# Kernel optimization log

Measured on AMD Instinct MI355X. Metric: run time of the kernel, lower is better.

The kernel has to match this reference:

```python
import jax, jax.numpy as jnp
from jax import lax
import numpy as np

B, C_IN, C_OUT, T, N, E = 4, 32, 32, 48, 2000, 16000


def _tconv(x, w, b):
    # Conv2d with kernel (3,1), padding (1,0): temporal conv over T, per-node.
    y = lax.conv_general_dilated(x, w, window_strides=(1, 1),
                                 padding=((1, 1), (0, 0)),
                                 dimension_numbers=('NCHW', 'OIHW', 'NCHW'))
    return y + b[None, :, None, None]


def setup_inputs() -> dict:
    key = jax.random.key(0)
    ks = jax.random.split(key, 8)
    x = jax.random.normal(ks[0], (B, C_IN, T, N), dtype=jnp.float32)
    edge_index = jax.random.randint(ks[1], (2, E), 0, N, dtype=jnp.int64)
    w1 = jax.random.normal(ks[2], (C_OUT, C_IN, 3, 1), dtype=jnp.float32) * 0.05
    b1 = jnp.zeros((C_OUT,), dtype=jnp.float32)
    gcn_w = jax.random.normal(ks[3], (C_OUT, C_OUT), dtype=jnp.float32) * 0.05
    gcn_b = jnp.zeros((C_OUT,), dtype=jnp.float32)
    w2 = jax.random.normal(ks[4], (C_OUT, C_OUT, 3, 1), dtype=jnp.float32) * 0.05
    b2 = jnp.zeros((C_OUT,), dtype=jnp.float32)
    return {"x": x, "edge_index": edge_index, "w1": w1, "b1": b1,
            "gcn_w": gcn_w, "gcn_b": gcn_b, "w2": w2, "b2": b2}


def reference(x, edge_index, w1, b1, gcn_w, gcn_b, w2, b2):
    # temporal conv 1 + relu
    h = jax.nn.relu(_tconv(x, w1, b1))          # [B, C, T, N]
    Bs, C, Ts, Ns = h.shape
    # replicate-graph GCN: same edge_index for all B*T graphs
    xf = h.transpose(0, 2, 3, 1).reshape(Bs * Ts, Ns, C)   # [BT, N, C]
    xw = xf @ gcn_w                                        # linear transform first
    src, dst = edge_index[0], edge_index[1]
    # GCN symmetric normalization with self-loops: deg = 1 + in-degree
    deg = jnp.zeros((Ns,), xw.dtype).at[dst].add(1.0) + 1.0
    dinv = lax.rsqrt(deg)
    wedge = dinv[src] * dinv[dst]                           # [E]

    def aggregate(g):  # g: [N, C] for one graph
        return jnp.zeros((Ns, C), g.dtype).at[dst].add(g[src] * wedge[:, None])

    agg = jax.vmap(aggregate)(xw)                           # [BT, N, C]
    out = agg + (1.0 / deg)[None, :, None] * xw + gcn_b     # self-loop term + bias
    out = out.reshape(Bs, Ts, Ns, C).transpose(0, 3, 1, 2)  # [B, C, T, N]
    # temporal conv 2
    return _tconv(out, w2, b2)
```

## Files before the change

kernel.cpp:

```cpp
#include <hip/hip_runtime.h>

#define BB 4
#define CIN 32
#define COUT 32
#define TT 48
#define NN 2000
#define EE 16000
#define BT (BB*TT)
#define PADCOL 24576


__global__ __launch_bounds__(1024) void k_build(
        const int* __restrict__ ei,
        const float* __restrict__ w1, const float* __restrict__ gw,
        const float* __restrict__ gb, const float* __restrict__ w2,
        int* __restrict__ rowptr, float* __restrict__ dinv2,
        float* __restrict__ dinvg, int* __restrict__ fillptr,
        int* __restrict__ col, float* __restrict__ wedge,
        float* __restrict__ w1t, float* __restrict__ w2c,
        float* __restrict__ bias2) {
    __shared__ int   cnt[2048];
    __shared__ int   buf[2048];
    __shared__ float sw2t[3072];
    __shared__ float sgw[1024];
    int t = threadIdx.x;

    for (int i = t; i < 3072; i += 1024) {
        int c = i & 31, r = i >> 5;
        int co = r & 31, k = r >> 5;
        sw2t[i] = w2[c * 96 + co * 3 + k];
        w1t[i]  = w1[c * 96 + co * 3 + k];
    }
    sgw[t] = gw[t];
    cnt[t] = 0; cnt[t + 1024] = 0;
    __syncthreads();

    for (int e = t; e < EE; e += 1024) atomicAdd(&cnt[ei[EE + e]], 1);
    __syncthreads();

    for (int i = t; i < 2048; i += 1024)
        buf[i] = (i < NN) ? ((cnt[i] + 3) & ~3) : 0;
    __syncthreads();
    for (int s = 1; s < 2048; s <<= 1) {
        int i0 = t, i1 = t + 1024;
        int a0 = buf[i0] + ((i0 >= s) ? buf[i0 - s] : 0);
        int a1 = buf[i1] + ((i1 >= s) ? buf[i1 - s] : 0);
        __syncthreads();
        buf[i0] = a0; buf[i1] = a1;
        __syncthreads();
    }

    for (int i = t; i < 2048; i += 1024) {
        if (i < NN) {
            rowptr[i + 1] = buf[i];
            float deg = (float)(cnt[i] + 1);
            dinvg[i] = rsqrtf(deg);
            dinv2[i] = 1.0f / deg;
            fillptr[i] = buf[i] - ((cnt[i] + 3) & ~3);
        }
    }
    if (t == 0) rowptr[0] = 0;

    int P = buf[NN - 1];
    __syncthreads();
    for (int i = t; i < P; i += 1024) { col[i] = 0; wedge[i] = 0.f; }

    for (int i = t; i < 3072; i += 1024) {
        int c = i & 31, r = i >> 5;
        int cm = r & 31, k = r >> 5;
        float acc = 0.f;
#pragma unroll
        for (int co = 0; co < 32; co++)
            acc += sgw[cm * 32 + co] * sw2t[(k * 32 + co) * 32 + c];
        w2c[i] = acc;
    }
    for (int i = t; i < 96; i += 1024) {
        int k = i >> 5, c = i & 31;
        float acc = 0.f;
#pragma unroll
        for (int co = 0; co < 32; co++)
            acc += gb[co] * sw2t[(k * 32 + co) * 32 + c];
        bias2[i] = acc;
    }
}


__global__ void k_fill(const int* __restrict__ ei, int* __restrict__ fillptr,
                       const float* __restrict__ dinvg,
                       int* __restrict__ col, float* __restrict__ wedge) {
    int e = blockIdx.x * blockDim.x + threadIdx.x;
    if (e < EE) {
        int s = ei[e], d = ei[EE + e];
        int pos = atomicAdd(fillptr + d, 1);
        col[pos]   = s;
        wedge[pos] = dinvg[s] * dinvg[d];
    }
}


__global__ __launch_bounds__(256) void k_conv1(const float* __restrict__ x,
                                               const float* __restrict__ w1t,
                                               const float* __restrict__ b1,
                                               float* __restrict__ hbuf) {
    int bid = blockIdx.x;
    int xcd = bid & 7;
    int i   = bid >> 3;
    int nch = i & 7;
    int r   = i >> 3;
    int tloc = r % 6, b = r / 6;
    int t = xcd * 6 + tloc;
    int n = nch * 256 + threadIdx.x;
    if (n >= NN) return;
    int g = b * TT + t;
    int gb = g >> 3, gsub = g & 7;

    float ha[COUT];
#pragma unroll
    for (int c = 0; c < COUT; c++) ha[c] = b1[c];

    for (int k = 0; k < 3; k++) {
        int tt = t + k - 1;
        if (tt < 0 || tt >= TT) continue;
        const float* xb = x + (((size_t)b * CIN) * TT + tt) * NN + n;

        float xv[CIN];
#pragma unroll
        for (int ci = 0; ci < CIN; ci++)
            xv[ci] = xb[(size_t)ci * TT * NN];
        __builtin_amdgcn_sched_barrier(0);

        const float* wp = w1t + k * CIN * COUT;
#pragma unroll
        for (int ci = 0; ci < CIN; ci++) {
#pragma unroll
            for (int c = 0; c < COUT; c++) ha[c] += xv[ci] * wp[ci * COUT + c];
        }
        __builtin_amdgcn_sched_barrier(0);
    }

    float4* pa = (float4*)(hbuf + (((size_t)gb * NN + n) * 8 + gsub) * 32);
#pragma unroll
    for (int q = 0; q < 8; q++)
        pa[q] = make_float4(fmaxf(ha[4*q], 0.f), fmaxf(ha[4*q+1], 0.f),
                            fmaxf(ha[4*q+2], 0.f), fmaxf(ha[4*q+3], 0.f));
}


__global__ __launch_bounds__(256) void k_agg(const float* __restrict__ hbuf,
                                             const int* __restrict__ rowptr,
                                             const int* __restrict__ col,
                                             const float* __restrict__ wedge,
                                             const float* __restrict__ dinv2,
                                             float* __restrict__ gbuf) {
    int bid = blockIdx.x;
    int xcd = bid & 7;
    int q   = bid >> 3;
    int gbr = q / 500;
    int nch = q % 500;
    int gb  = gbr * 8 + xcd;
    int wid  = threadIdx.x >> 6;
    int lane = threadIdx.x & 63;
    int gsub = lane >> 3;
    int cq   = lane & 7;
    int n    = nch * 4 + wid;

    const float* xg = hbuf + (size_t)gb * NN * 256;
    size_t loff = (size_t)gsub * 32 + cq * 4;

    float4 self = *(const float4*)(xg + (size_t)n * 256 + loff);
    float dv = dinv2[n];
    float4 acc = make_float4(dv * self.x, dv * self.y, dv * self.z, dv * self.w);

    int j  = rowptr[n];
    int je = rowptr[n + 1];
    for (; j < je; j += 4) {
        int4   cc = *(const int4*)(col + j);
        float4 ww = *(const float4*)(wedge + j);
        float4 v0 = *(const float4*)(xg + (size_t)cc.x * 256 + loff);
        float4 v1 = *(const float4*)(xg + (size_t)cc.y * 256 + loff);
        float4 v2 = *(const float4*)(xg + (size_t)cc.z * 256 + loff);
        float4 v3 = *(const float4*)(xg + (size_t)cc.w * 256 + loff);
        acc.x += ww.x*v0.x + ww.y*v1.x + ww.z*v2.x + ww.w*v3.x;
        acc.y += ww.x*v0.y + ww.y*v1.y + ww.z*v2.y + ww.w*v3.y;
        acc.z += ww.x*v0.z + ww.y*v1.z + ww.z*v2.z + ww.w*v3.z;
        acc.w += ww.x*v0.w + ww.y*v1.w + ww.z*v2.w + ww.w*v3.w;
    }

    int g = gb * 8 + gsub;
    *(float4*)(gbuf + ((size_t)g * NN + n) * 32 + cq * 4) = acc;
}


__global__ __launch_bounds__(256) void k_conv2(const float* __restrict__ gbuf,
                                               const float* __restrict__ w2c,
                                               const float* __restrict__ bias2,
                                               const float* __restrict__ b2,
                                               float* __restrict__ out) {
    int n = blockIdx.x * 256 + threadIdx.x;
    if (n >= NN) return;
    int t = blockIdx.y, b = blockIdx.z;

    float o[COUT];
#pragma unroll
    for (int c = 0; c < COUT; c++) o[c] = b2[c];

    for (int k = 0; k < 3; k++) {
        int tt = t + k - 1;
        if (tt < 0 || tt >= TT) continue;
        const float4* gp = (const float4*)(gbuf + (((size_t)(b * TT + tt)) * NN + n) * CIN);
        const float* wp = w2c + k * CIN * COUT;
        const float* bp = bias2 + k * COUT;
        float gv[CIN];
#pragma unroll
        for (int qq = 0; qq < 8; qq++) {
            float4 v = gp[qq];
            gv[4*qq] = v.x; gv[4*qq+1] = v.y; gv[4*qq+2] = v.z; gv[4*qq+3] = v.w;
        }
#pragma unroll
        for (int c = 0; c < COUT; c++) o[c] += bp[c];
#pragma unroll
        for (int cm = 0; cm < CIN; cm++) {
#pragma unroll
            for (int c = 0; c < COUT; c++) o[c] += gv[cm] * wp[cm * COUT + c];
        }
    }

#pragma unroll
    for (int c = 0; c < COUT; c++)
        out[(((size_t)b * COUT + c) * TT + t) * NN + n] = o[c];
}


extern "C" void kernel_launch(void* const* d_in, const int* in_sizes, int n_in,
                              void* d_out, int out_size, void* d_ws, size_t ws_size,
                              hipStream_t stream) {
    const float* x     = (const float*)d_in[0];
    const int*   ei    = (const int*)d_in[1];
    const float* w1    = (const float*)d_in[2];
    const float* b1    = (const float*)d_in[3];
    const float* gcn_w = (const float*)d_in[4];
    const float* gcn_b = (const float*)d_in[5];
    const float* w2    = (const float*)d_in[6];
    const float* b2    = (const float*)d_in[7];
    float* out = (float*)d_out;

    const size_t XWB = (size_t)BT * NN * COUT * sizeof(float);
    char* w = (char*)d_ws;
    float* hbuf    = (float*)w;  w += XWB;
    float* gbuf    = (float*)w;  w += XWB;
    int*   rowptr  = (int*)w;    w += 8192;
    float* dinv2   = (float*)w;  w += 8192;
    float* dinvg   = (float*)w;  w += 8192;
    int*   fillptr = (int*)w;    w += 8192;
    int*   col     = (int*)w;    w += PADCOL * sizeof(int);
    float* wedge   = (float*)w;  w += PADCOL * sizeof(float);
    float* w1t     = (float*)w;  w += 3072 * sizeof(float);
    float* w2c     = (float*)w;  w += 3072 * sizeof(float);
    float* bias2   = (float*)w;  w += 96 * sizeof(float);

    k_build<<<dim3(1), dim3(1024), 0, stream>>>(ei, w1, gcn_w, gcn_b, w2,
                                                rowptr, dinv2, dinvg, fillptr,
                                                col, wedge, w1t, w2c, bias2);
    k_fill <<<dim3((EE + 255) / 256), dim3(256), 0, stream>>>(ei, fillptr, dinvg, col, wedge);
    k_conv1<<<dim3(1536), dim3(256), 0, stream>>>(x, w1t, b1, hbuf);
    k_agg  <<<dim3(12000), dim3(256), 0, stream>>>(hbuf, rowptr, col, wedge, dinv2, gbuf);
    k_conv2<<<dim3(8, TT, BB), dim3(256), 0, stream>>>(gbuf, w2c, bias2, b2, out);
}
```

Baseline: 248.4 us.

## Compute two output timesteps per thread in conv2 with shared tap loads

Each conv2 thread now produces two adjacent output timesteps, so the four gbuf input timesteps are loaded once and reused across both outputs instead of loading three taps per output. Bias contributions are precomputed into three boundary classes in k_build, and the grid is flattened with an XCD-aware block mapping plus sched_barriers to interleave loads and FMAs. This cuts gbuf traffic by about a third, at the cost of higher register pressure from two 32-wide accumulators and two 32-wide input buffers.

```diff
diff --git a/kernel.cpp b/kernel.cpp
--- a/kernel.cpp
+++ b/kernel.cpp
@@ -14,15 +14,17 @@
         const int* __restrict__ ei,
         const float* __restrict__ w1, const float* __restrict__ gw,
         const float* __restrict__ gb, const float* __restrict__ w2,
+        const float* __restrict__ cb2,
         int* __restrict__ rowptr, float* __restrict__ dinv2,
         float* __restrict__ dinvg, int* __restrict__ fillptr,
         int* __restrict__ col, float* __restrict__ wedge,
         float* __restrict__ w1t, float* __restrict__ w2c,
-        float* __restrict__ bias2) {
+        float* __restrict__ biasE) {
     __shared__ int   cnt[2048];
     __shared__ int   buf[2048];
     __shared__ float sw2t[3072];
     __shared__ float sgw[1024];
+    __shared__ float sbk[96];
     int t = threadIdx.x;
 
     for (int i = t; i < 3072; i += 1024) {
@@ -80,7 +82,15 @@
 #pragma unroll
         for (int co = 0; co < 32; co++)
             acc += gb[co] * sw2t[(k * 32 + co) * 32 + c];
-        bias2[i] = acc;
+        sbk[i] = acc;
+    }
+    __syncthreads();
+    for (int i = t; i < 96; i += 1024) {
+        int cls = i >> 5, c = i & 31;
+        float v = cb2[c] + sbk[32 + c];
+        if (cls != 0) v += sbk[c];
+        if (cls != 2) v += sbk[64 + c];
+        biasE[i] = v;
     }
 }
 
@@ -191,43 +201,79 @@
 }
 
 
-__global__ __launch_bounds__(256) void k_conv2(const float* __restrict__ gbuf,
-                                               const float* __restrict__ w2c,
-                                               const float* __restrict__ bias2,
-                                               const float* __restrict__ b2,
-                                               float* __restrict__ out) {
-    int n = blockIdx.x * 256 + threadIdx.x;
+#define LOADTAP(GV, TIDX) { \
+    const float4* gp_ = (const float4*)(gbuf + (((size_t)(b * TT + (TIDX))) * NN + n) * 32); \
+    _Pragma("unroll") \
+    for (int q_ = 0; q_ < 8; q_++) { \
+        float4 v_ = gp_[q_]; \
+        GV[4*q_] = v_.x; GV[4*q_+1] = v_.y; GV[4*q_+2] = v_.z; GV[4*q_+3] = v_.w; } }
+
+#define KBLK(ACC, GV, WP) { \
+    _Pragma("unroll") \
+    for (int cm_ = 0; cm_ < 32; cm_++) { \
+        float g_ = GV[cm_]; \
+        _Pragma("unroll") \
+        for (int c_ = 0; c_ < 32; c_++) ACC[c_] += g_ * (WP)[cm_ * 32 + c_]; } }
+
+#define STOREACC(ACC, TOUT, BP) { \
+    _Pragma("unroll") \
+    for (int c_ = 0; c_ < 32; c_++) \
+        out[(((size_t)b * COUT + c_) * TT + (TOUT)) * NN + n] = ACC[c_] + (BP)[c_]; }
+
+__global__ __launch_bounds__(256, 3) void k_conv2(const float* __restrict__ gbuf,
+                                                  const float* __restrict__ w2c,
+                                                  const float* __restrict__ biasE,
+                                                  float* __restrict__ out) {
+    int bid  = blockIdx.x;
+    int xcd  = bid & 7;
+    int slot = bid >> 3;
+    int grp  = xcd * 12 + (slot >> 3);
+    int nch  = slot & 7;
+    int b  = grp / 24;
+    int tc = grp % 24;
+    int t0 = tc * 2;
+    int n  = nch * 256 + threadIdx.x;
     if (n >= NN) return;
-    int t = blockIdx.y, b = blockIdx.z;
-
-    float o[COUT];
-#pragma unroll
-    for (int c = 0; c < COUT; c++) o[c] = b2[c];
-
-    for (int k = 0; k < 3; k++) {
-        int tt = t + k - 1;
-        if (tt < 0 || tt >= TT) continue;
-        const float4* gp = (const float4*)(gbuf + (((size_t)(b * TT + tt)) * NN + n) * CIN);
-        const float* wp = w2c + k * CIN * COUT;
-        const float* bp = bias2 + k * COUT;
-        float gv[CIN];
-#pragma unroll
-        for (int qq = 0; qq < 8; qq++) {
-            float4 v = gp[qq];
-            gv[4*qq] = v.x; gv[4*qq+1] = v.y; gv[4*qq+2] = v.z; gv[4*qq+3] = v.w;
-        }
-#pragma unroll
-        for (int c = 0; c < COUT; c++) o[c] += bp[c];
-#pragma unroll
-        for (int cm = 0; cm < CIN; cm++) {
-#pragma unroll
-            for (int c = 0; c < COUT; c++) o[c] += gv[cm] * wp[cm * COUT + c];
-        }
-    }
-
-#pragma unroll
-    for (int c = 0; c < COUT; c++)
-        out[(((size_t)b * COUT + c) * TT + t) * NN + n] = o[c];
+
+    const float* W0 = w2c;
+    const float* W1 = w2c + 1024;
+    const float* W2 = w2c + 2048;
+
+    float acc0[COUT], acc1[COUT];
+#pragma unroll
+    for (int c = 0; c < COUT; c++) { acc0[c] = 0.f; acc1[c] = 0.f; }
+
+    float ga[CIN], gbv[CIN];
+
+    if (t0 > 0) LOADTAP(ga, t0 - 1);
+    LOADTAP(gbv, t0);
+    __builtin_amdgcn_sched_barrier(0);
+
+    if (t0 > 0) { KBLK(acc0, ga, W0); }
+    __builtin_amdgcn_sched_barrier(0);
+
+    LOADTAP(ga, t0 + 1);
+    __builtin_amdgcn_sched_barrier(0);
+
+    KBLK(acc0, gbv, W1);
+    KBLK(acc1, gbv, W0);
+    __builtin_amdgcn_sched_barrier(0);
+
+    if (t0 + 2 < TT) LOADTAP(gbv, t0 + 2);
+    __builtin_amdgcn_sched_barrier(0);
+
+    KBLK(acc0, ga, W2);
+    int cls0 = (t0 == 0) ? 0 : 1;
+    const float* bp0 = biasE + cls0 * 32;
+    STOREACC(acc0, t0, bp0);
+
+    KBLK(acc1, ga, W1);
+    __builtin_amdgcn_sched_barrier(0);
+
+    if (t0 + 2 < TT) { KBLK(acc1, gbv, W2); }
+    int cls1 = (t0 + 1 == TT - 1) ? 2 : 1;
+    const float* bp1 = biasE + cls1 * 32;
+    STOREACC(acc1, t0 + 1, bp1);
 }
 
 
@@ -256,13 +302,13 @@
     float* wedge   = (float*)w;  w += PADCOL * sizeof(float);
     float* w1t     = (float*)w;  w += 3072 * sizeof(float);
     float* w2c     = (float*)w;  w += 3072 * sizeof(float);
-    float* bias2   = (float*)w;  w += 96 * sizeof(float);
-
-    k_build<<<dim3(1), dim3(1024), 0, stream>>>(ei, w1, gcn_w, gcn_b, w2,
+    float* biasE   = (float*)w;  w += 96 * sizeof(float);
+
+    k_build<<<dim3(1), dim3(1024), 0, stream>>>(ei, w1, gcn_w, gcn_b, w2, b2,
                                                 rowptr, dinv2, dinvg, fillptr,
-                                                col, wedge, w1t, w2c, bias2);
+                                                col, wedge, w1t, w2c, biasE);
     k_fill <<<dim3((EE + 255) / 256), dim3(256), 0, stream>>>(ei, fillptr, dinvg, col, wedge);
     k_conv1<<<dim3(1536), dim3(256), 0, stream>>>(x, w1t, b1, hbuf);
     k_agg  <<<dim3(12000), dim3(256), 0, stream>>>(hbuf, rowptr, col, wedge, dinv2, gbuf);
-    k_conv2<<<dim3(8, TT, BB), dim3(256), 0, stream>>>(gbuf, w2c, bias2, b2, out);
-}
+    k_conv2<<<dim3(768), dim3(256), 0, stream>>>(gbuf, w2c, biasE, out);
+}
```

Measured after the change: 392.9 us. +58.2%, slower.
